# Kernel tuning notes

Hardware: AMD Instinct MI355X
Metric: run time of the kernel (lower is better)

## Reference

```python
import jax, jax.numpy as jnp
import numpy as np

NUM_HEADS = 16
EMBED_DIM = 1024
B, L = 1, 4096


def setup_inputs() -> dict:
    key = jax.random.key(0)
    k1, k2, k3 = jax.random.split(key, 3)
    x = jax.random.normal(k1, (B, L, EMBED_DIM), dtype=jnp.float32)
    # torch nn.Linear weights are [out_features, in_features]
    w_attn = jax.random.normal(k2, (3 * EMBED_DIM, EMBED_DIM), dtype=jnp.float32) * (EMBED_DIM ** -0.5)
    w_proj = jax.random.normal(k3, (EMBED_DIM, EMBED_DIM), dtype=jnp.float32) * (EMBED_DIM ** -0.5)
    return {"x": x, "w_attn": w_attn, "w_proj": w_proj}


def reference(x, w_attn, w_proj):
    b, l, e = x.shape
    h = NUM_HEADS
    hd = e // h
    qkv = x @ w_attn.T                      # [B, L, 3E]
    q, k, v = jnp.split(qkv, 3, axis=-1)
    # [B, H, L, hd]
    q = q.reshape(b, l, h, hd).transpose(0, 2, 1, 3)
    k = k.reshape(b, l, h, hd).transpose(0, 2, 1, 3)
    v = v.reshape(b, l, h, hd).transpose(0, 2, 1, 3)
    scale = 1.0 / jnp.sqrt(jnp.asarray(hd, dtype=x.dtype))
    scores = jnp.einsum('bhld,bhsd->bhls', q, k) * scale  # [B, H, L, L]
    causal = jnp.tril(jnp.ones((l, l), dtype=bool))
    scores = jnp.where(causal, scores, jnp.asarray(-jnp.inf, dtype=scores.dtype))
    attn = jax.nn.softmax(scores, axis=-1)
    y = jnp.einsum('bhls,bhsd->bhld', attn, v)            # [B, H, L, hd]
    y = y.transpose(0, 2, 1, 3).reshape(b, l, e)
    return y @ w_proj.T
```

## Files before the change

### kernel.cpp

```cpp
#include <hip/hip_runtime.h>

#define LSEQ 4096
#define EMB  1024
#define NH   16
#define HD   64

typedef __attribute__((ext_vector_type(8)))  __bf16 bf16x8;
typedef __attribute__((ext_vector_type(4)))  float f32x4;
typedef __attribute__((ext_vector_type(16))) float f32x16;
typedef __attribute__((ext_vector_type(8)))  unsigned short u16x8;
typedef __attribute__((ext_vector_type(4)))  unsigned short u16x4;
typedef __attribute__((ext_vector_type(4)))  unsigned int u32x4;

__device__ __forceinline__ unsigned short f2bf(float f) {
    union { float f; unsigned u; } v; v.f = f;
    unsigned r = v.u + 0x7fffu + ((v.u >> 16) & 1u);
    return (unsigned short)(r >> 16);
}

__device__ __forceinline__ unsigned cvt_pk_bf16(float a, float b) {
    unsigned r;
    asm("v_cvt_pk_bf16_f32 %0, %1, %2" : "=v"(r) : "v"(a), "v"(b));
    return r;
}

__device__ __forceinline__ void plswap(unsigned &x, unsigned &y) {
    asm volatile("v_permlane32_swap_b32 %0, %1" : "+v"(x), "+v"(y));
}

__device__ __forceinline__ f32x4 mfma16(u16x8 a, u16x8 b, f32x4 c) {
    return __builtin_amdgcn_mfma_f32_16x16x32_bf16(
        __builtin_bit_cast(bf16x8, a), __builtin_bit_cast(bf16x8, b), c, 0, 0, 0);
}

__device__ __forceinline__ f32x16 mfma32(u16x8 a, u16x8 b, f32x16 c) {
    return __builtin_amdgcn_mfma_f32_32x32x16_bf16(
        __builtin_bit_cast(bf16x8, a), __builtin_bit_cast(bf16x8, b), c, 0, 0, 0);
}

__device__ __forceinline__ void gload16(const void* g, void* l) {
    __builtin_amdgcn_global_load_lds((const __attribute__((address_space(1))) unsigned int*)g,
                                     (__attribute__((address_space(3))) unsigned int*)l,
                                     16, 0, 0);
}

#define NXC (LSEQ * EMB / 4)
#define NAC (3 * EMB * EMB / 4)
#define NPC (EMB * EMB / 4)
__global__ __launch_bounds__(256) void cvt_all(const float* __restrict__ x,
                                               const float* __restrict__ wa,
                                               const float* __restrict__ wp,
                                               unsigned short* __restrict__ out) {
    int i = blockIdx.x * 256 + threadIdx.x;
    if (i >= NXC + NAC + NPC) return;
    const float* src;
    if (i < NXC)             src = x + (size_t)i * 4;
    else if (i < NXC + NAC)  src = wa + (size_t)(i - NXC) * 4;
    else                     src = wp + (size_t)(i - NXC - NAC) * 4;
    f32x4 v = *(const f32x4*)src;
    u16x4 o;
    o[0] = f2bf(v[0]); o[1] = f2bf(v[1]); o[2] = f2bf(v[2]); o[3] = f2bf(v[3]);
    *(u16x4*)(out + (size_t)i * 4) = o;
}

__global__ __launch_bounds__(256, 2) void gemm_qkv(const unsigned short* __restrict__ A,
                                                   const unsigned short* __restrict__ B,
                                                   unsigned short* __restrict__ Qo,
                                                   unsigned short* __restrict__ Ko,
                                                   unsigned short* __restrict__ Vto) {
    __shared__ unsigned short As[128 * 32];
    __shared__ unsigned short Bs[128 * 32];
    const int tid = threadIdx.x;
    const int lane = tid & 63;
    const int wv = tid >> 6;
    const int wm = wv >> 1, wn = wv & 1;
    const int li = lane & 15, g = lane >> 4;
    const int m0 = blockIdx.y * 128, n0 = blockIdx.x * 128;
    f32x4 acc[4][4] = {};
    for (int k0 = 0; k0 < EMB; k0 += 32) {
        #pragma unroll
        for (int c = 0; c < 2; ++c) {
            const int o = c * 4096 + tid * 16;
            const int r = o >> 6, cb = o & 63;
            gload16((const char*)A + ((size_t)(m0 + r) * EMB + k0) * 2 + cb, (char*)As + o);
            gload16((const char*)B + ((size_t)(n0 + r) * EMB + k0) * 2 + cb, (char*)Bs + o);
        }
        __syncthreads();
        u16x8 af[4], bfr[4];
        #pragma unroll
        for (int mb = 0; mb < 4; ++mb)
            af[mb] = *(const u16x8*)(As + (wm * 64 + mb * 16 + li) * 32 + g * 8);
        #pragma unroll
        for (int nb = 0; nb < 4; ++nb)
            bfr[nb] = *(const u16x8*)(Bs + (wn * 64 + nb * 16 + li) * 32 + g * 8);
        #pragma unroll
        for (int mb = 0; mb < 4; ++mb)
            #pragma unroll
            for (int nb = 0; nb < 4; ++nb)
                acc[mb][nb] = mfma16(af[mb], bfr[nb], acc[mb][nb]);
        __syncthreads();
    }
    for (int mb = 0; mb < 4; ++mb) {
        for (int nb = 0; nb < 4; ++nb) {
            for (int r = 0; r < 4; ++r) {
                const int m = m0 + wm * 64 + mb * 16 + g * 4 + r;
                const int n = n0 + wn * 64 + nb * 16 + li;
                const float v = acc[mb][nb][r];
                if (n < EMB) {
                    Qo[((size_t)(n >> 6) * LSEQ + m) * HD + (n & 63)] = f2bf(v * 0.1803368801111244f);
                } else if (n < 2 * EMB) {
                    const int c = n - EMB;
                    Ko[((size_t)(c >> 6) * LSEQ + m) * HD + (c & 63)] = f2bf(v);
                } else {
                    const int c = n - 2 * EMB;
                    Vto[((size_t)(c >> 6) * HD + (c & 63)) * LSEQ + m] = f2bf(v);
                }
            }
        }
    }
}

__global__ __launch_bounds__(256, 2) void attn_fwd(const unsigned short* __restrict__ Q,
                                                   const unsigned short* __restrict__ K,
                                                   const unsigned short* __restrict__ Vt,
                                                   unsigned short* __restrict__ Y) {
    __shared__ char LB[2][32768];
    const int d0 = blockIdx.x;
    const int grp = d0 & 255;
    const int head = 2 * (grp & 7) + ((grp >> 3) & 1);
    const int t16 = grp >> 4;
    const int s = (d0 < 256) ? (31 - t16) : t16;
    const int tid = threadIdx.x, lane = tid & 63, w = tid >> 6;
    const int li = lane & 31, hf = lane >> 5;
    const int qw0 = s * 128 + w * 32;
    const int qrow = qw0 + li;
    const int jmaxw = 2 * s + (w >> 1);
    const int nst = s + 1;
    const char* KhB = (const char*)(K + (size_t)head * LSEQ * HD);
    const char* VhB = (const char*)(Vt + (size_t)head * HD * LSEQ);

    u16x8 bq[4];
    #pragma unroll
    for (int ks = 0; ks < 4; ++ks)
        bq[ks] = *(const u16x8*)(Q + ((size_t)head * LSEQ + qrow) * HD + ks * 16 + hf * 8);

    int off[4];
    #pragma unroll
    for (int ks = 0; ks < 4; ++ks) {
        const int c = 2 * ks + hf;
        off[ks] = c * 1024 + (((li & 24) | ((li & 7) ^ c)) << 4);
    }

    const int row0 = tid >> 3, sch = tid & 7;
    const int wd0 = sch * 1024 + (((row0 & 24) | ((row0 & 7) ^ sch)) << 4);

    u16x8 kr[4], vr[4];
    #define LOADKV(js_) do {                                                              \
        const char* kp_ = KhB + ((size_t)((js_) * 128 + row0)) * 128 + sch * 16;          \
        const char* vp_ = VhB + (size_t)row0 * (LSEQ * 2) + (js_) * 256 + sch * 16;       \
        kr[0] = *(const u16x8*)kp_;                                                       \
        kr[1] = *(const u16x8*)(kp_ + 32 * 128);                                          \
        kr[2] = *(const u16x8*)(kp_ + 64 * 128);                                          \
        kr[3] = *(const u16x8*)(kp_ + 96 * 128);                                          \
        vr[0] = *(const u16x8*)vp_;                                                       \
        vr[1] = *(const u16x8*)(vp_ + (size_t)32 * (LSEQ * 2));                           \
        vr[2] = *(const u16x8*)(vp_ + 128);                                               \
        vr[3] = *(const u16x8*)(vp_ + (size_t)32 * (LSEQ * 2) + 128);                     \
    } while (0)
    #define WRITEKV(b_) do {                                                              \
        char* base_ = LB[b_];                                                             \
        *(u16x8*)(base_ + wd0)                     = kr[0];                               \
        *(u16x8*)(base_ + wd0 + 512)               = kr[1];                               \
        *(u16x8*)(base_ + 8192 + wd0)              = kr[2];                               \
        *(u16x8*)(base_ + 8192 + wd0 + 512)        = kr[3];                               \
        *(u16x8*)(base_ + 16384 + wd0)             = vr[0];                               \
        *(u16x8*)(base_ + 16384 + wd0 + 512)       = vr[1];                               \
        *(u16x8*)(base_ + 24576 + wd0)             = vr[2];                               \
        *(u16x8*)(base_ + 24576 + wd0 + 512)       = vr[3];                               \
    } while (0)

    float l_i = 0.f;
    f32x16 oA = {}, oB = {};

    LOADKV(0);
    WRITEKV(0);
    __syncthreads();
    for (int js = 0; js < nst; ++js) {
        const int cur = js & 1;
        if (js + 1 < nst) LOADKV(js + 1);
        #pragma unroll
        for (int c = 0; c < 2; ++c) {
            const int j = 2 * js + c;
            if (j <= jmaxw) {
                const char* Kb = LB[cur] + c * 8192;
                const char* Vb = LB[cur] + 16384 + c * 8192;
                f32x16 sA = {}, sB = {};
                __builtin_amdgcn_s_setprio(1);
                #pragma unroll
                for (int ks = 0; ks < 4; ++ks) {
                    const u16x8 ka0 = *(const u16x8*)(Kb + off[ks]);
                    const u16x8 ka1 = *(const u16x8*)(Kb + off[ks] + 512);
                    sA = mfma32(ka0, bq[ks], sA);
                    sB = mfma32(ka1, bq[ks], sB);
                }
                __builtin_amdgcn_s_setprio(0);
                if (j == jmaxw && (j * 64 + 63 > qw0)) {
                    const int kbase = j * 64;
                    #pragma unroll
                    for (int r = 0; r < 16; ++r) {
                        const int kvl = kbase + (r & 3) + 8 * (r >> 2) + 4 * hf;
                        if (kvl > qrow)      sA[r] = -1e30f;
                        if (kvl + 32 > qrow) sB[r] = -1e30f;
                    }
                }
                float s0 = 0.f, s1 = 0.f;
                unsigned uA[8], uB[8];
                #pragma unroll
                for (int wd = 0; wd < 8; ++wd) {
                    const float a0 = __builtin_amdgcn_exp2f(sA[2 * wd]);
                    const float a1 = __builtin_amdgcn_exp2f(sA[2 * wd + 1]);
                    const float b0 = __builtin_amdgcn_exp2f(sB[2 * wd]);
                    const float b1 = __builtin_amdgcn_exp2f(sB[2 * wd + 1]);
                    s0 += a0 + a1; s1 += b0 + b1;
                    uA[wd] = cvt_pk_bf16(a0, a1);
                    uB[wd] = cvt_pk_bf16(b0, b1);
                }
                l_i += s0 + s1;
                plswap(uA[0], uA[2]); plswap(uA[1], uA[3]);
                plswap(uA[4], uA[6]); plswap(uA[5], uA[7]);
                plswap(uB[0], uB[2]); plswap(uB[1], uB[3]);
                plswap(uB[4], uB[6]); plswap(uB[5], uB[7]);
                const u32x4 wA0 = {uA[0], uA[1], uA[2], uA[3]};
                const u32x4 wA1 = {uA[4], uA[5], uA[6], uA[7]};
                const u32x4 wB0 = {uB[0], uB[1], uB[2], uB[3]};
                const u32x4 wB1 = {uB[4], uB[5], uB[6], uB[7]};
                const u16x8 ap0 = __builtin_bit_cast(u16x8, wA0);
                const u16x8 ap1 = __builtin_bit_cast(u16x8, wA1);
                const u16x8 ap2 = __builtin_bit_cast(u16x8, wB0);
                const u16x8 ap3 = __builtin_bit_cast(u16x8, wB1);
                const u16x8 va0 = *(const u16x8*)(Vb + off[0]);
                const u16x8 va1 = *(const u16x8*)(Vb + off[1]);
                const u16x8 va2 = *(const u16x8*)(Vb + off[2]);
                const u16x8 va3 = *(const u16x8*)(Vb + off[3]);
                const u16x8 vc0 = *(const u16x8*)(Vb + off[0] + 512);
                const u16x8 vc1 = *(const u16x8*)(Vb + off[1] + 512);
                const u16x8 vc2 = *(const u16x8*)(Vb + off[2] + 512);
                const u16x8 vc3 = *(const u16x8*)(Vb + off[3] + 512);
                __builtin_amdgcn_s_setprio(1);
                oA = mfma32(ap0, va0, oA);
                oA = mfma32(ap1, va1, oA);
                oA = mfma32(ap2, va2, oA);
                oA = mfma32(ap3, va3, oA);
                oB = mfma32(ap0, vc0, oB);
                oB = mfma32(ap1, vc1, oB);
                oB = mfma32(ap2, vc2, oB);
                oB = mfma32(ap3, vc3, oB);
                __builtin_amdgcn_s_setprio(0);
            }
        }
        if (js + 1 < nst) WRITEKV(cur ^ 1);
        __syncthreads();
    }
    #undef LOADKV
    #undef WRITEKV
    const float lt = l_i + __shfl_xor(l_i, 32);
    const float linv = 1.0f / lt;
    #pragma unroll
    for (int r = 0; r < 16; ++r) {
        const int ql = (r & 3) + 8 * (r >> 2) + 4 * hf;
        const float gl = __shfl(linv, ql);
        Y[(size_t)(qw0 + ql) * EMB + head * HD + li]      = f2bf(oA[r] * gl);
        Y[(size_t)(qw0 + ql) * EMB + head * HD + 32 + li] = f2bf(oB[r] * gl);
    }
}

__global__ __launch_bounds__(256, 2) void gemm_proj(const unsigned short* __restrict__ A,
                                                    const unsigned short* __restrict__ B,
                                                    float* __restrict__ C) {
    __shared__ unsigned short As[128 * 32];
    __shared__ unsigned short Bs[128 * 32];
    const int tid = threadIdx.x;
    const int lane = tid & 63;
    const int wv = tid >> 6;
    const int wm = wv >> 1, wn = wv & 1;
    const int li = lane & 15, g = lane >> 4;
    const int m0 = blockIdx.y * 128, n0 = blockIdx.x * 128;
    f32x4 acc[4][4] = {};
    for (int k0 = 0; k0 < EMB; k0 += 32) {
        #pragma unroll
        for (int c = 0; c < 2; ++c) {
            const int o = c * 4096 + tid * 16;
            const int r = o >> 6, cb = o & 63;
            gload16((const char*)A + ((size_t)(m0 + r) * EMB + k0) * 2 + cb, (char*)As + o);
            gload16((const char*)B + ((size_t)(n0 + r) * EMB + k0) * 2 + cb, (char*)Bs + o);
        }
        __syncthreads();
        u16x8 af[4], bfr[4];
        #pragma unroll
        for (int mb = 0; mb < 4; ++mb)
            af[mb] = *(const u16x8*)(As + (wm * 64 + mb * 16 + li) * 32 + g * 8);
        #pragma unroll
        for (int nb = 0; nb < 4; ++nb)
            bfr[nb] = *(const u16x8*)(Bs + (wn * 64 + nb * 16 + li) * 32 + g * 8);
        #pragma unroll
        for (int mb = 0; mb < 4; ++mb)
            #pragma unroll
            for (int nb = 0; nb < 4; ++nb)
                acc[mb][nb] = mfma16(af[mb], bfr[nb], acc[mb][nb]);
        __syncthreads();
    }
    for (int mb = 0; mb < 4; ++mb)
        for (int nb = 0; nb < 4; ++nb)
            for (int r = 0; r < 4; ++r) {
                const int m = m0 + wm * 64 + mb * 16 + g * 4 + r;
                const int n = n0 + wn * 64 + nb * 16 + li;
                C[(size_t)m * EMB + n] = acc[mb][nb][r];
            }
}

extern "C" void kernel_launch(void* const* d_in, const int* in_sizes, int n_in,
                              void* d_out, int out_size, void* d_ws, size_t ws_size,
                              hipStream_t stream) {
    const float* x      = (const float*)d_in[0];
    const float* w_attn = (const float*)d_in[1];
    const float* w_proj = (const float*)d_in[2];
    float* out = (float*)d_out;

    unsigned short* ws  = (unsigned short*)d_ws;
    unsigned short* xb  = ws;
    unsigned short* wab = xb + (size_t)LSEQ * EMB;
    unsigned short* wpb = wab + (size_t)3 * EMB * EMB;
    unsigned short* Qb  = wpb + (size_t)EMB * EMB;
    unsigned short* Kb  = Qb + (size_t)LSEQ * EMB;
    unsigned short* Vtb = Kb + (size_t)LSEQ * EMB;
    unsigned short* Yb  = Vtb + (size_t)LSEQ * EMB;

    const int ntot = NXC + NAC + NPC;
    cvt_all<<<(ntot + 255) / 256, 256, 0, stream>>>(x, w_attn, w_proj, xb);
    gemm_qkv<<<dim3(3 * EMB / 128, LSEQ / 128), 256, 0, stream>>>(xb, wab, Qb, Kb, Vtb);
    attn_fwd<<<dim3(512), 256, 0, stream>>>(Qb, Kb, Vtb, Yb);
    gemm_proj<<<dim3(EMB / 128, LSEQ / 128), 256, 0, stream>>>(Yb, wpb, out);
}
```

Measured before the change: 135.2 us.

## Split KV sub-tiles across two wave groups in attention and merge partial outputs

Measured after the change: 126.2 us. 6.6% less time.

```diff
diff --git a/kernel.cpp b/kernel.cpp
--- a/kernel.cpp
+++ b/kernel.cpp
@@ -120,7 +120,7 @@
     }
 }
 
-__global__ __launch_bounds__(256, 2) void attn_fwd(const unsigned short* __restrict__ Q,
+__global__ __launch_bounds__(512, 4) void attn_fwd(const unsigned short* __restrict__ Q,
                                                    const unsigned short* __restrict__ K,
                                                    const unsigned short* __restrict__ Vt,
                                                    unsigned short* __restrict__ Y) {
@@ -131,10 +131,11 @@
     const int t16 = grp >> 4;
     const int s = (d0 < 256) ? (31 - t16) : t16;
     const int tid = threadIdx.x, lane = tid & 63, w = tid >> 6;
+    const int qs = w & 3, par = w >> 2;
     const int li = lane & 31, hf = lane >> 5;
-    const int qw0 = s * 128 + w * 32;
+    const int qw0 = s * 128 + qs * 32;
     const int qrow = qw0 + li;
-    const int jmaxw = 2 * s + (w >> 1);
+    const int jmaxw = 2 * s + (qs >> 1);
     const int nst = s + 1;
     const char* KhB = (const char*)(K + (size_t)head * LSEQ * HD);
     const char* VhB = (const char*)(Vt + (size_t)head * HD * LSEQ);
@@ -151,32 +152,24 @@
         off[ks] = c * 1024 + (((li & 24) | ((li & 7) ^ c)) << 4);
     }
 
-    const int row0 = tid >> 3, sch = tid & 7;
+    const int row0 = (tid >> 3) & 31, sch = tid & 7, half = tid >> 8;
     const int wd0 = sch * 1024 + (((row0 & 24) | ((row0 & 7) ^ sch)) << 4);
 
-    u16x8 kr[4], vr[4];
+    u16x8 kr0, kr1, vr0, vr1;
     #define LOADKV(js_) do {                                                              \
-        const char* kp_ = KhB + ((size_t)((js_) * 128 + row0)) * 128 + sch * 16;          \
-        const char* vp_ = VhB + (size_t)row0 * (LSEQ * 2) + (js_) * 256 + sch * 16;       \
-        kr[0] = *(const u16x8*)kp_;                                                       \
-        kr[1] = *(const u16x8*)(kp_ + 32 * 128);                                          \
-        kr[2] = *(const u16x8*)(kp_ + 64 * 128);                                          \
-        kr[3] = *(const u16x8*)(kp_ + 96 * 128);                                          \
-        vr[0] = *(const u16x8*)vp_;                                                       \
-        vr[1] = *(const u16x8*)(vp_ + (size_t)32 * (LSEQ * 2));                           \
-        vr[2] = *(const u16x8*)(vp_ + 128);                                               \
-        vr[3] = *(const u16x8*)(vp_ + (size_t)32 * (LSEQ * 2) + 128);                     \
+        const char* kp_ = KhB + ((size_t)((js_) * 128 + half * 64 + row0)) * 128 + sch * 16; \
+        const char* vp_ = VhB + (size_t)row0 * (LSEQ * 2) + ((js_) * 128 + half * 64) * 2 + sch * 16; \
+        kr0 = *(const u16x8*)kp_;                                                         \
+        kr1 = *(const u16x8*)(kp_ + 32 * 128);                                            \
+        vr0 = *(const u16x8*)vp_;                                                         \
+        vr1 = *(const u16x8*)(vp_ + (size_t)32 * (LSEQ * 2));                             \
     } while (0)
     #define WRITEKV(b_) do {                                                              \
-        char* base_ = LB[b_];                                                             \
-        *(u16x8*)(base_ + wd0)                     = kr[0];                               \
-        *(u16x8*)(base_ + wd0 + 512)               = kr[1];                               \
-        *(u16x8*)(base_ + 8192 + wd0)              = kr[2];                               \
-        *(u16x8*)(base_ + 8192 + wd0 + 512)        = kr[3];                               \
-        *(u16x8*)(base_ + 16384 + wd0)             = vr[0];                               \
-        *(u16x8*)(base_ + 16384 + wd0 + 512)       = vr[1];                               \
-        *(u16x8*)(base_ + 24576 + wd0)             = vr[2];                               \
-        *(u16x8*)(base_ + 24576 + wd0 + 512)       = vr[3];                               \
+        char* base_ = LB[b_] + half * 8192;                                               \
+        *(u16x8*)(base_ + wd0)               = kr0;                                       \
+        *(u16x8*)(base_ + wd0 + 512)         = kr1;                                       \
+        *(u16x8*)(base_ + 16384 + wd0)       = vr0;                                       \
+        *(u16x8*)(base_ + 16384 + wd0 + 512) = vr1;                                       \
     } while (0)
 
     float l_i = 0.f;
@@ -188,89 +181,105 @@
     for (int js = 0; js < nst; ++js) {
         const int cur = js & 1;
         if (js + 1 < nst) LOADKV(js + 1);
-        #pragma unroll
-        for (int c = 0; c < 2; ++c) {
-            const int j = 2 * js + c;
-            if (j <= jmaxw) {
-                const char* Kb = LB[cur] + c * 8192;
-                const char* Vb = LB[cur] + 16384 + c * 8192;
-                f32x16 sA = {}, sB = {};
-                __builtin_amdgcn_s_setprio(1);
+        const int j = 2 * js + par;
+        if (j <= jmaxw) {
+            const char* Kb = LB[cur] + par * 8192;
+            const char* Vb = LB[cur] + 16384 + par * 8192;
+            f32x16 sA = {}, sB = {};
+            __builtin_amdgcn_s_setprio(1);
+            #pragma unroll
+            for (int ks = 0; ks < 4; ++ks) {
+                const u16x8 ka0 = *(const u16x8*)(Kb + off[ks]);
+                const u16x8 ka1 = *(const u16x8*)(Kb + off[ks] + 512);
+                sA = mfma32(ka0, bq[ks], sA);
+                sB = mfma32(ka1, bq[ks], sB);
+            }
+            __builtin_amdgcn_s_setprio(0);
+            if (j == jmaxw && (j * 64 + 63 > qw0)) {
+                const int kbase = j * 64;
                 #pragma unroll
-                for (int ks = 0; ks < 4; ++ks) {
-                    const u16x8 ka0 = *(const u16x8*)(Kb + off[ks]);
-                    const u16x8 ka1 = *(const u16x8*)(Kb + off[ks] + 512);
-                    sA = mfma32(ka0, bq[ks], sA);
-                    sB = mfma32(ka1, bq[ks], sB);
+                for (int r = 0; r < 16; ++r) {
+                    const int kvl = kbase + (r & 3) + 8 * (r >> 2) + 4 * hf;
+                    if (kvl > qrow)      sA[r] = -1e30f;
+                    if (kvl + 32 > qrow) sB[r] = -1e30f;
                 }
-                __builtin_amdgcn_s_setprio(0);
-                if (j == jmaxw && (j * 64 + 63 > qw0)) {
-                    const int kbase = j * 64;
-                    #pragma unroll
-                    for (int r = 0; r < 16; ++r) {
-                        const int kvl = kbase + (r & 3) + 8 * (r >> 2) + 4 * hf;
-                        if (kvl > qrow)      sA[r] = -1e30f;
-                        if (kvl + 32 > qrow) sB[r] = -1e30f;
-                    }
-                }
-                float s0 = 0.f, s1 = 0.f;
-                unsigned uA[8], uB[8];
-                #pragma unroll
-                for (int wd = 0; wd < 8; ++wd) {
-                    const float a0 = __builtin_amdgcn_exp2f(sA[2 * wd]);
-                    const float a1 = __builtin_amdgcn_exp2f(sA[2 * wd + 1]);
-                    const float b0 = __builtin_amdgcn_exp2f(sB[2 * wd]);
-                    const float b1 = __builtin_amdgcn_exp2f(sB[2 * wd + 1]);
-                    s0 += a0 + a1; s1 += b0 + b1;
-                    uA[wd] = cvt_pk_bf16(a0, a1);
-                    uB[wd] = cvt_pk_bf16(b0, b1);
-                }
-                l_i += s0 + s1;
-                plswap(uA[0], uA[2]); plswap(uA[1], uA[3]);
-                plswap(uA[4], uA[6]); plswap(uA[5], uA[7]);
-                plswap(uB[0], uB[2]); plswap(uB[1], uB[3]);
-                plswap(uB[4], uB[6]); plswap(uB[5], uB[7]);
-                const u32x4 wA0 = {uA[0], uA[1], uA[2], uA[3]};
-                const u32x4 wA1 = {uA[4], uA[5], uA[6], uA[7]};
-                const u32x4 wB0 = {uB[0], uB[1], uB[2], uB[3]};
-                const u32x4 wB1 = {uB[4], uB[5], uB[6], uB[7]};
-                const u16x8 ap0 = __builtin_bit_cast(u16x8, wA0);
-                const u16x8 ap1 = __builtin_bit_cast(u16x8, wA1);
-                const u16x8 ap2 = __builtin_bit_cast(u16x8, wB0);
-                const u16x8 ap3 = __builtin_bit_cast(u16x8, wB1);
-                const u16x8 va0 = *(const u16x8*)(Vb + off[0]);
-                const u16x8 va1 = *(const u16x8*)(Vb + off[1]);
-                const u16x8 va2 = *(const u16x8*)(Vb + off[2]);
-                const u16x8 va3 = *(const u16x8*)(Vb + off[3]);
-                const u16x8 vc0 = *(const u16x8*)(Vb + off[0] + 512);
-                const u16x8 vc1 = *(const u16x8*)(Vb + off[1] + 512);
-                const u16x8 vc2 = *(const u16x8*)(Vb + off[2] + 512);
-                const u16x8 vc3 = *(const u16x8*)(Vb + off[3] + 512);
-                __builtin_amdgcn_s_setprio(1);
-                oA = mfma32(ap0, va0, oA);
-                oA = mfma32(ap1, va1, oA);
-                oA = mfma32(ap2, va2, oA);
-                oA = mfma32(ap3, va3, oA);
-                oB = mfma32(ap0, vc0, oB);
-                oB = mfma32(ap1, vc1, oB);
-                oB = mfma32(ap2, vc2, oB);
-                oB = mfma32(ap3, vc3, oB);
-                __builtin_amdgcn_s_setprio(0);
-            }
+            }
+            float s0 = 0.f, s1 = 0.f;
+            unsigned uA[8], uB[8];
+            #pragma unroll
+            for (int wd = 0; wd < 8; ++wd) {
+                const float a0 = __builtin_amdgcn_exp2f(sA[2 * wd]);
+                const float a1 = __builtin_amdgcn_exp2f(sA[2 * wd + 1]);
+                const float b0 = __builtin_amdgcn_exp2f(sB[2 * wd]);
+                const float b1 = __builtin_amdgcn_exp2f(sB[2 * wd + 1]);
+                s0 += a0 + a1; s1 += b0 + b1;
+                uA[wd] = cvt_pk_bf16(a0, a1);
+                uB[wd] = cvt_pk_bf16(b0, b1);
+            }
+            l_i += s0 + s1;
+            plswap(uA[0], uA[2]); plswap(uA[1], uA[3]);
+            plswap(uA[4], uA[6]); plswap(uA[5], uA[7]);
+            plswap(uB[0], uB[2]); plswap(uB[1], uB[3]);
+            plswap(uB[4], uB[6]); plswap(uB[5], uB[7]);
+            const u32x4 wA0 = {uA[0], uA[1], uA[2], uA[3]};
+            const u32x4 wA1 = {uA[4], uA[5], uA[6], uA[7]};
+            const u32x4 wB0 = {uB[0], uB[1], uB[2], uB[3]};
+            const u32x4 wB1 = {uB[4], uB[5], uB[6], uB[7]};
+            const u16x8 ap0 = __builtin_bit_cast(u16x8, wA0);
+            const u16x8 ap1 = __builtin_bit_cast(u16x8, wA1);
+            const u16x8 ap2 = __builtin_bit_cast(u16x8, wB0);
+            const u16x8 ap3 = __builtin_bit_cast(u16x8, wB1);
+            const u16x8 va0 = *(const u16x8*)(Vb + off[0]);
+            const u16x8 va1 = *(const u16x8*)(Vb + off[1]);
+            const u16x8 va2 = *(const u16x8*)(Vb + off[2]);
+            const u16x8 va3 = *(const u16x8*)(Vb + off[3]);
+            const u16x8 vc0 = *(const u16x8*)(Vb + off[0] + 512);
+            const u16x8 vc1 = *(const u16x8*)(Vb + off[1] + 512);
+            const u16x8 vc2 = *(const u16x8*)(Vb + off[2] + 512);
+            const u16x8 vc3 = *(const u16x8*)(Vb + off[3] + 512);
+            __builtin_amdgcn_s_setprio(1);
+            oA = mfma32(ap0, va0, oA);
+            oA = mfma32(ap1, va1, oA);
+            oA = mfma32(ap2, va2, oA);
+            oA = mfma32(ap3, va3, oA);
+            oB = mfma32(ap0, vc0, oB);
+            oB = mfma32(ap1, vc1, oB);
+            oB = mfma32(ap2, vc2, oB);
+            oB = mfma32(ap3, vc3, oB);
+            __builtin_amdgcn_s_setprio(0);
         }
         if (js + 1 < nst) WRITEKV(cur ^ 1);
         __syncthreads();
     }
     #undef LOADKV
     #undef WRITEKV
-    const float lt = l_i + __shfl_xor(l_i, 32);
-    const float linv = 1.0f / lt;
-    #pragma unroll
-    for (int r = 0; r < 16; ++r) {
-        const int ql = (r & 3) + 8 * (r >> 2) + 4 * hf;
-        const float gl = __shfl(linv, ql);
-        Y[(size_t)(qw0 + ql) * EMB + head * HD + li]      = f2bf(oA[r] * gl);
-        Y[(size_t)(qw0 + ql) * EMB + head * HD + 32 + li] = f2bf(oB[r] * gl);
+    if (par == 1) {
+        float* po = (float*)(LB[0] + qs * 8192);
+        #pragma unroll
+        for (int r = 0; r < 16; ++r) {
+            po[r * 64 + lane]        = oA[r];
+            po[(16 + r) * 64 + lane] = oB[r];
+        }
+        ((float*)LB[1])[qs * 64 + lane] = l_i;
+    }
+    __syncthreads();
+    if (par == 0) {
+        const float* po = (const float*)(LB[0] + qs * 8192);
+        l_i += ((const float*)LB[1])[qs * 64 + lane];
+        #pragma unroll
+        for (int r = 0; r < 16; ++r) {
+            oA[r] += po[r * 64 + lane];
+            oB[r] += po[(16 + r) * 64 + lane];
+        }
+        const float lt = l_i + __shfl_xor(l_i, 32);
+        const float linv = 1.0f / lt;
+        #pragma unroll
+        for (int r = 0; r < 16; ++r) {
+            const int ql = (r & 3) + 8 * (r >> 2) + 4 * hf;
+            const float gl = __shfl(linv, ql);
+            Y[(size_t)(qw0 + ql) * EMB + head * HD + li]      = f2bf(oA[r] * gl);
+            Y[(size_t)(qw0 + ql) * EMB + head * HD + 32 + li] = f2bf(oB[r] * gl);
+        }
     }
 }
 
@@ -338,6 +347,6 @@
     const int ntot = NXC + NAC + NPC;
     cvt_all<<<(ntot + 255) / 256, 256, 0, stream>>>(x, w_attn, w_proj, xb);
     gemm_qkv<<<dim3(3 * EMB / 128, LSEQ / 128), 256, 0, stream>>>(xb, wab, Qb, Kb, Vtb);
-    attn_fwd<<<dim3(512), 256, 0, stream>>>(Qb, Kb, Vtb, Yb);
+    attn_fwd<<<dim3(512), 512, 0, stream>>>(Qb, Kb, Vtb, Yb);
     gemm_proj<<<dim3(EMB / 128, LSEQ / 128), 256, 0, stream>>>(Yb, wpb, out);
 }
```
